# Performance work log

Hardware: AMD Instinct MI355X
Metric: run time of the kernel (lower is better)

The kernel has to match this reference:

```python
import jax, jax.numpy as jnp
import numpy as np

B_CAPS = 32   # number of capsule types
K = 3         # kernel size
P = 4         # pose matrix side
STRIDE = 2
ITERS = 3
PSIZE = P * P
LN_2PI = np.float32(np.log(2.0 * np.pi))


def setup_inputs() -> dict:
    key = jax.random.key(0)
    k1, k2, k3, k4, k5 = jax.random.split(key, 5)
    b, h, w = 32, 32, 32
    x = jax.random.normal(k1, (b, h, w, B_CAPS, PSIZE), jnp.float32)
    a = jax.random.uniform(k2, (b, h, w, B_CAPS, 1), jnp.float32)
    # learned params (torch: weights (1,1,1,K*K,B,P,P), beta_u/beta_a (B,1))
    weights = jax.random.normal(k3, (K * K, B_CAPS, P, P), jnp.float32)
    beta_u = 0.1 * jax.random.normal(k4, (B_CAPS, 1), jnp.float32)
    beta_a = 0.1 * jax.random.normal(k5, (B_CAPS, 1), jnp.float32)
    return {"x": x, "a": a, "weights": weights, "beta_u": beta_u, "beta_a": beta_a}


def _patch(t):
    # t: (b, h, w, B, psize) -> (b, oh, ow, K*K, B, psize)
    b, h, w = t.shape[0], t.shape[1], t.shape[2]
    starts = np.arange(0, h - K + 1, STRIDE)
    idxs = starts[:, None] + np.arange(K)[None, :]          # (oh, K) static gather indices
    oh = idxs.shape[0]
    t = t[:, idxs]                                           # (b, oh, K, w, B, ps)
    t = t[:, :, :, idxs]                                     # (b, oh, K, ow, K, B, ps)
    t = jnp.transpose(t, (0, 1, 3, 2, 4, 5, 6))              # (b, oh, ow, K, K, B, ps)
    return t.reshape(b, oh, oh, K * K, t.shape[-2], t.shape[-1]), oh


def _em_routing(v, a_in, beta_u, beta_a):
    # v: (b,h,w,Bk,C,psize)  a_in: (b,h,w,Bk,C)   Bk = K*K, C = B_CAPS
    eps = 1e-6
    lam = 1e-3
    b, h, w, Bk, C, ps = v.shape
    mu = sigma_sq = a_out = None
    for it in range(ITERS):
        if it == 0:
            r = a_in / C                                                    # (b,h,w,Bk,C)
        else:
            ln_pjh = (-(v - mu) ** 2 / (2.0 * sigma_sq)
                      - jnp.log(jnp.sqrt(sigma_sq)) - 0.5 * LN_2PI)         # (b,h,w,Bk,C,ps)
            ln_ap = ln_pjh.sum(axis=5) + jnp.log(a_out.reshape(b, h, w, 1, C))
            r = jax.nn.softmax(ln_ap, axis=4)
        r_sum = r.sum(axis=3, keepdims=True)                                # (b,h,w,1,C)
        coeff = (r / (r_sum + eps))[..., None]                              # (b,h,w,Bk,C,1)
        mu = jnp.sum(coeff * v, axis=3, keepdims=True)                      # (b,h,w,1,C,ps)
        sigma_sq = jnp.sum(coeff * (v - mu) ** 2, axis=3, keepdims=True) + eps
        cost_h = (beta_u + jnp.log(jnp.sqrt(sigma_sq))) * r_sum[..., None]  # (b,h,w,1,C,ps)
        a_out = jax.nn.sigmoid(lam * (beta_a - cost_h.sum(axis=5, keepdims=True)))
    return mu.reshape(b, h, w, C, ps), a_out.reshape(b, h, w, C, 1)


def reference(x, a, weights, beta_u, beta_a):
    b = x.shape[0]
    p_in, oh = _patch(x)                                    # (b,oh,ow,K*K,B,psize)
    a_in, _ = _patch(a)                                     # (b,oh,ow,K*K,B,1)
    p = p_in.reshape(b, oh, oh, K * K, B_CAPS, P, P)
    # voting: per-window, per-type 4x4 pose matmul
    v = jnp.einsum('bhwkcpq,kcqr->bhwkcpr', p, weights).reshape(b, oh, oh, K * K, B_CAPS, PSIZE)
    a_in = a_in.reshape(b, oh, oh, K * K, B_CAPS)
    return _em_routing(v, a_in, beta_u, beta_a)
```

## Files before the change

### kernel.cpp

```cpp
#include <hip/hip_runtime.h>
#include <math.h>

#define PP 9
#define CAPS 32
#define PS 16
#define OH 15
#define HH 32
#define WW 32
#define LN_2PI 1.8378770664093453f

typedef float f32x2 __attribute__((ext_vector_type(2)));

__device__ __forceinline__ float frcp(float x) {
    float r;
    asm("v_rcp_f32 %0, %1" : "=v"(r) : "v"(x));
    return r;
}
__device__ __forceinline__ f32x2 splat2(float x) {
    f32x2 r; r.x = x; r.y = x; return r;
}
__device__ __forceinline__ f32x2 pkfma(f32x2 a, f32x2 b, f32x2 c) {
    return __builtin_elementwise_fma(a, b, c);
}

template <int CTRL>
__device__ __forceinline__ float dppf(float x) {
    int r = __builtin_amdgcn_update_dpp(0, __builtin_bit_cast(int, x), CTRL, 0xF, 0xF, true);
    return __builtin_bit_cast(float, r);
}
__device__ __forceinline__ float row_sum16(float x) {
    x += dppf<0xB1>(x);
    x += dppf<0x4E>(x);
    x += dppf<0x124>(x);
    x += dppf<0x128>(x);
    return x;
}
__device__ __forceinline__ float row_max16(float x) {
    x = fmaxf(x, dppf<0xB1>(x));
    x = fmaxf(x, dppf<0x4E>(x));
    x = fmaxf(x, dppf<0x124>(x));
    x = fmaxf(x, dppf<0x128>(x));
    return x;
}
__device__ __forceinline__ float swz_xor16(float x) {
    return __builtin_bit_cast(float,
        __builtin_amdgcn_ds_swizzle(__builtin_bit_cast(int, x), 0x401F));
}

__global__ __launch_bounds__(64, 2) void emcaps_kernel(
    const float* __restrict__ x,
    const float* __restrict__ a,
    const float* __restrict__ wgt,
    const float* __restrict__ beta_u,
    const float* __restrict__ beta_a,
    float* __restrict__ out_mu,
    float* __restrict__ out_a)
{
    const int lane = threadIdx.x;
    const int s = lane >> 5;
    const int c = lane & 31;

    const int site = blockIdx.x * 2 + s;
    const int j = site % OH;
    const int t2 = site / OH;
    const int i = t2 % OH;
    const int b = t2 / OH;
    const int h0 = 2 * i, w0 = 2 * j;

    f32x2 v[PP][8];
    float r[PP];
    #pragma unroll
    for (int k = 0; k < PP; ++k) {
        const int hh = h0 + k / 3, ww = w0 + k % 3;
        const size_t pix = (size_t)(b * HH + hh) * WW + ww;
        const float* xb = x + pix * (CAPS * PS) + c * PS;
        *(float4*)&v[k][0] = *(const float4*)xb;
        *(float4*)&v[k][2] = *(const float4*)(xb + 4);
        *(float4*)&v[k][4] = *(const float4*)(xb + 8);
        *(float4*)&v[k][6] = *(const float4*)(xb + 12);
        r[k] = a[pix * CAPS + c] * (1.f / 32.f);
    }

    #pragma unroll
    for (int k = 0; k < PP; ++k) {
        float xt[PS];
        #pragma unroll
        for (int m = 0; m < 8; ++m) { xt[2 * m] = v[k][m].x; xt[2 * m + 1] = v[k][m].y; }
        f32x2 w2[8];
        const float* wb = wgt + k * (CAPS * PS) + c * PS;
        *(float4*)&w2[0] = *(const float4*)wb;
        *(float4*)&w2[2] = *(const float4*)(wb + 4);
        *(float4*)&w2[4] = *(const float4*)(wb + 8);
        *(float4*)&w2[6] = *(const float4*)(wb + 12);
        #pragma unroll
        for (int m = 0; m < 8; ++m) {
            f32x2 acc = splat2(0.f);
            #pragma unroll
            for (int q = 0; q < 4; ++q)
                acc = pkfma(splat2(xt[4 * (m >> 1) + q]), w2[q * 2 + (m & 1)], acc);
            v[k][m] = acc;
        }
    }

    const float bu = beta_u[c];
    const float ba = beta_a[c];
    const float eps = 1e-6f;
    const float lam = 1e-3f;

    f32x2 mu2[8], is22[8];
    float aoc = 0.f;
    float slgfull = 0.f;
    float r_sum;

    for (int it = 0; it < 3; ++it) {
        if (it > 0) {
            const float addc = __logf(aoc) - slgfull - 8.f * LN_2PI;
            #pragma unroll
            for (int k = 0; k < PP; ++k) {
                f32x2 s2 = splat2(0.f);
                #pragma unroll
                for (int m = 0; m < 8; ++m) {
                    f32x2 d = v[k][m] - mu2[m];
                    s2 = pkfma(d * d, is22[m], s2);
                }
                const float sacc = s2.x + s2.y;
                const float lnk = addc - sacc;
                float mx = row_max16(lnk);
                mx = fmaxf(mx, swz_xor16(mx));
                float e = __expf(lnk - mx);
                float ss = row_sum16(e);
                ss += swz_xor16(ss);
                r[k] = e * frcp(ss);
            }
        }

        r_sum = 0.f;
        #pragma unroll
        for (int k = 0; k < PP; ++k) r_sum += r[k];
        const float invr = frcp(r_sum + eps);
        f32x2 rr[PP];
        #pragma unroll
        for (int k = 0; k < PP; ++k) { r[k] *= invr; rr[k] = splat2(r[k]); }

        #pragma unroll
        for (int m = 0; m < 8; ++m) {
            f32x2 acc = splat2(0.f);
            #pragma unroll
            for (int k = 0; k < PP; ++k) acc = pkfma(rr[k], v[k][m], acc);
            mu2[m] = acc;
        }
        float slg = 0.f;
        #pragma unroll
        for (int m = 0; m < 8; ++m) {
            f32x2 acc = splat2(0.f);
            #pragma unroll
            for (int k = 0; k < PP; ++k) {
                f32x2 d = v[k][m] - mu2[m];
                acc = pkfma(rr[k] * d, d, acc);
            }
            f32x2 sg = acc + splat2(eps);
            is22[m].x = frcp(2.f * sg.x);
            is22[m].y = frcp(2.f * sg.y);
            slg += 0.5f * __logf(sg.x * sg.y);
        }
        slgfull = slg;
        const float ch = r_sum * (16.f * bu + slgfull);
        aoc = frcp(1.f + __expf(-lam * (ba - ch)));
    }

    float* ob = out_mu + (size_t)site * (CAPS * PS) + c * PS;
    *(float4*)(ob + 0)  = *(float4*)&mu2[0];
    *(float4*)(ob + 4)  = *(float4*)&mu2[2];
    *(float4*)(ob + 8)  = *(float4*)&mu2[4];
    *(float4*)(ob + 12) = *(float4*)&mu2[6];
    out_a[(size_t)site * CAPS + c] = aoc;
}

extern "C" void kernel_launch(void* const* d_in, const int* in_sizes, int n_in,
                              void* d_out, int out_size, void* d_ws, size_t ws_size,
                              hipStream_t stream) {
    const float* x      = (const float*)d_in[0];
    const float* a      = (const float*)d_in[1];
    const float* wgt    = (const float*)d_in[2];
    const float* beta_u = (const float*)d_in[3];
    const float* beta_a = (const float*)d_in[4];

    float* out_mu = (float*)d_out;
    float* out_a  = (float*)d_out + (size_t)32 * OH * OH * CAPS * PS;

    const int n_sites = 32 * OH * OH;
    emcaps_kernel<<<n_sites / 2, 64, 0, stream>>>(x, a, wgt, beta_u, beta_a, out_mu, out_a);
}
```

Baseline: 38.20 us.

## Split each routing site's nine kernel positions across two wave halves

Each 64-lane block now handles one output site, with the two 32-lane halves each owning up to five of the nine kernel positions. Partial sums for r_sum, mu and sigma are combined across halves via xor-32 shuffles, and a padded slot is masked out. This cuts per-thread register state and doubles the grid to raise occupancy and latency hiding. In exchange it duplicates the per-capsule routing math in both halves and adds cross-half shuffle latency.

```diff
diff --git a/kernel.cpp b/kernel.cpp
--- a/kernel.cpp
+++ b/kernel.cpp
@@ -2,6 +2,7 @@
 #include <math.h>
 
 #define PP 9
+#define NK 5
 #define CAPS 32
 #define PS 16
 #define OH 15
@@ -46,8 +47,14 @@
     return __builtin_bit_cast(float,
         __builtin_amdgcn_ds_swizzle(__builtin_bit_cast(int, x), 0x401F));
 }
-
-__global__ __launch_bounds__(64, 2) void emcaps_kernel(
+__device__ __forceinline__ float xhalf(float x) {
+    return __shfl_xor(x, 32);
+}
+__device__ __forceinline__ f32x2 xhalf2(f32x2 x) {
+    f32x2 r; r.x = __shfl_xor(x.x, 32); r.y = __shfl_xor(x.y, 32); return r;
+}
+
+__global__ __launch_bounds__(64, 3) void emcaps_kernel(
     const float* __restrict__ x,
     const float* __restrict__ a,
     const float* __restrict__ wgt,
@@ -57,48 +64,60 @@
     float* __restrict__ out_a)
 {
     const int lane = threadIdx.x;
-    const int s = lane >> 5;
+    const int half = lane >> 5;
     const int c = lane & 31;
 
-    const int site = blockIdx.x * 2 + s;
+    const int site = blockIdx.x;
     const int j = site % OH;
     const int t2 = site / OH;
     const int i = t2 % OH;
     const int b = t2 / OH;
     const int h0 = 2 * i, w0 = 2 * j;
 
-    f32x2 v[PP][8];
-    float r[PP];
+    const float kmask = half ? 0.f : 1.f;
+
+    f32x2 v[NK][8];
+    float r[NK];
     #pragma unroll
-    for (int k = 0; k < PP; ++k) {
-        const int hh = h0 + k / 3, ww = w0 + k % 3;
-        const size_t pix = (size_t)(b * HH + hh) * WW + ww;
-        const float* xb = x + pix * (CAPS * PS) + c * PS;
-        *(float4*)&v[k][0] = *(const float4*)xb;
-        *(float4*)&v[k][2] = *(const float4*)(xb + 4);
-        *(float4*)&v[k][4] = *(const float4*)(xb + 8);
-        *(float4*)&v[k][6] = *(const float4*)(xb + 12);
-        r[k] = a[pix * CAPS + c] * (1.f / 32.f);
+    for (int kk = 0; kk < NK; ++kk) {
+        const int kg = half * NK + kk;
+        if (kg < PP) {
+            const int hh = h0 + kg / 3, ww = w0 + kg % 3;
+            const size_t pix = (size_t)(b * HH + hh) * WW + ww;
+            const float* xb = x + pix * (CAPS * PS) + c * PS;
+            *(float4*)&v[kk][0] = *(const float4*)xb;
+            *(float4*)&v[kk][2] = *(const float4*)(xb + 4);
+            *(float4*)&v[kk][4] = *(const float4*)(xb + 8);
+            *(float4*)&v[kk][6] = *(const float4*)(xb + 12);
+            r[kk] = a[pix * CAPS + c] * (1.f / 32.f);
+        } else {
+            #pragma unroll
+            for (int m = 0; m < 8; ++m) v[kk][m] = splat2(0.f);
+            r[kk] = 0.f;
+        }
     }
 
     #pragma unroll
-    for (int k = 0; k < PP; ++k) {
-        float xt[PS];
-        #pragma unroll
-        for (int m = 0; m < 8; ++m) { xt[2 * m] = v[k][m].x; xt[2 * m + 1] = v[k][m].y; }
-        f32x2 w2[8];
-        const float* wb = wgt + k * (CAPS * PS) + c * PS;
-        *(float4*)&w2[0] = *(const float4*)wb;
-        *(float4*)&w2[2] = *(const float4*)(wb + 4);
-        *(float4*)&w2[4] = *(const float4*)(wb + 8);
-        *(float4*)&w2[6] = *(const float4*)(wb + 12);
-        #pragma unroll
-        for (int m = 0; m < 8; ++m) {
-            f32x2 acc = splat2(0.f);
-            #pragma unroll
-            for (int q = 0; q < 4; ++q)
-                acc = pkfma(splat2(xt[4 * (m >> 1) + q]), w2[q * 2 + (m & 1)], acc);
-            v[k][m] = acc;
+    for (int kk = 0; kk < NK; ++kk) {
+        const int kg = half * NK + kk;
+        if (kg < PP) {
+            float xt[PS];
+            #pragma unroll
+            for (int m = 0; m < 8; ++m) { xt[2 * m] = v[kk][m].x; xt[2 * m + 1] = v[kk][m].y; }
+            f32x2 w2[8];
+            const float* wb = wgt + kg * (CAPS * PS) + c * PS;
+            *(float4*)&w2[0] = *(const float4*)wb;
+            *(float4*)&w2[2] = *(const float4*)(wb + 4);
+            *(float4*)&w2[4] = *(const float4*)(wb + 8);
+            *(float4*)&w2[6] = *(const float4*)(wb + 12);
+            #pragma unroll
+            for (int m = 0; m < 8; ++m) {
+                f32x2 acc = splat2(0.f);
+                #pragma unroll
+                for (int q = 0; q < 4; ++q)
+                    acc = pkfma(splat2(xt[4 * (m >> 1) + q]), w2[q * 2 + (m & 1)], acc);
+                v[kk][m] = acc;
+            }
         }
     }
 
@@ -116,49 +135,50 @@
         if (it > 0) {
             const float addc = __logf(aoc) - slgfull - 8.f * LN_2PI;
             #pragma unroll
-            for (int k = 0; k < PP; ++k) {
+            for (int kk = 0; kk < NK; ++kk) {
                 f32x2 s2 = splat2(0.f);
                 #pragma unroll
                 for (int m = 0; m < 8; ++m) {
-                    f32x2 d = v[k][m] - mu2[m];
+                    f32x2 d = v[kk][m] - mu2[m];
                     s2 = pkfma(d * d, is22[m], s2);
                 }
-                const float sacc = s2.x + s2.y;
-                const float lnk = addc - sacc;
+                const float lnk = addc - (s2.x + s2.y);
                 float mx = row_max16(lnk);
                 mx = fmaxf(mx, swz_xor16(mx));
                 float e = __expf(lnk - mx);
                 float ss = row_sum16(e);
                 ss += swz_xor16(ss);
-                r[k] = e * frcp(ss);
+                r[kk] = e * frcp(ss);
             }
-        }
-
-        r_sum = 0.f;
-        #pragma unroll
-        for (int k = 0; k < PP; ++k) r_sum += r[k];
+            r[NK - 1] *= kmask;
+        }
+
+        float rp = 0.f;
+        #pragma unroll
+        for (int kk = 0; kk < NK; ++kk) rp += r[kk];
+        r_sum = rp + xhalf(rp);
         const float invr = frcp(r_sum + eps);
-        f32x2 rr[PP];
-        #pragma unroll
-        for (int k = 0; k < PP; ++k) { r[k] *= invr; rr[k] = splat2(r[k]); }
+        f32x2 rr[NK];
+        #pragma unroll
+        for (int kk = 0; kk < NK; ++kk) { r[kk] *= invr; rr[kk] = splat2(r[kk]); }
 
         #pragma unroll
         for (int m = 0; m < 8; ++m) {
             f32x2 acc = splat2(0.f);
             #pragma unroll
-            for (int k = 0; k < PP; ++k) acc = pkfma(rr[k], v[k][m], acc);
-            mu2[m] = acc;
+            for (int kk = 0; kk < NK; ++kk) acc = pkfma(rr[kk], v[kk][m], acc);
+            mu2[m] = acc + xhalf2(acc);
         }
         float slg = 0.f;
         #pragma unroll
         for (int m = 0; m < 8; ++m) {
             f32x2 acc = splat2(0.f);
             #pragma unroll
-            for (int k = 0; k < PP; ++k) {
-                f32x2 d = v[k][m] - mu2[m];
-                acc = pkfma(rr[k] * d, d, acc);
+            for (int kk = 0; kk < NK; ++kk) {
+                f32x2 d = v[kk][m] - mu2[m];
+                acc = pkfma(rr[kk] * d, d, acc);
             }
-            f32x2 sg = acc + splat2(eps);
+            f32x2 sg = (acc + xhalf2(acc)) + splat2(eps);
             is22[m].x = frcp(2.f * sg.x);
             is22[m].y = frcp(2.f * sg.y);
             slg += 0.5f * __logf(sg.x * sg.y);
@@ -168,12 +188,14 @@
         aoc = frcp(1.f + __expf(-lam * (ba - ch)));
     }
 
-    float* ob = out_mu + (size_t)site * (CAPS * PS) + c * PS;
-    *(float4*)(ob + 0)  = *(float4*)&mu2[0];
-    *(float4*)(ob + 4)  = *(float4*)&mu2[2];
-    *(float4*)(ob + 8)  = *(float4*)&mu2[4];
-    *(float4*)(ob + 12) = *(float4*)&mu2[6];
-    out_a[(size_t)site * CAPS + c] = aoc;
+    if (half == 0) {
+        float* ob = out_mu + (size_t)site * (CAPS * PS) + c * PS;
+        *(float4*)(ob + 0)  = *(float4*)&mu2[0];
+        *(float4*)(ob + 4)  = *(float4*)&mu2[2];
+        *(float4*)(ob + 8)  = *(float4*)&mu2[4];
+        *(float4*)(ob + 12) = *(float4*)&mu2[6];
+        out_a[(size_t)site * CAPS + c] = aoc;
+    }
 }
 
 extern "C" void kernel_launch(void* const* d_in, const int* in_sizes, int n_in,
@@ -189,5 +211,5 @@
     float* out_a  = (float*)d_out + (size_t)32 * OH * OH * CAPS * PS;
 
     const int n_sites = 32 * OH * OH;
-    emcaps_kernel<<<n_sites / 2, 64, 0, stream>>>(x, a, wgt, beta_u, beta_a, out_mu, out_a);
-}
+    emcaps_kernel<<<n_sites, 64, 0, stream>>>(x, a, wgt, beta_u, beta_a, out_mu, out_a);
+}
```

After: 47.39 us. 1.24x slower.
